# Performance work log

Measured on AMD Instinct MI355X. Metric: run time of the kernel, lower is better.

The kernel has to match this reference:

```python
import jax, jax.numpy as jnp
import numpy as np

BETA = 0.25  # codebook loss weight


def setup_inputs() -> dict:
    key = jax.random.key(0)
    k1, k2 = jax.random.split(key)
    B, C, D = 32768, 4096, 128
    x = jax.random.normal(k1, (B, D), dtype=jnp.float32)
    codes = jax.random.normal(k2, (1, C, D), dtype=jnp.float32)
    return {"x": x, "codes": codes}


def reference(x, codes):
    # x: (B, D), codes: (1, C, D). l2 metric, spherical_norm=False, STE training path
    # (dead-code reinit branch is a no-op on first forward since unused_count==0).
    c = codes[0]  # (C, D)
    x_sq = jnp.sum(x * x, axis=-1, keepdims=True)           # (B, 1)
    c_sq = jnp.sum(c * c, axis=-1)                          # (C,)
    xc = jnp.einsum('bd,cd->bc', x, c)                      # (B, C)
    distances = x_sq + c_sq[None, :] - 2.0 * xc             # (B, C)
    indices = jnp.argmin(distances, axis=-1)                # (B,)
    quantized = c[indices]                                  # (B, D) codebook gather
    # straight-through estimator output
    quantized_out = x + jax.lax.stop_gradient(quantized - x)
    # loss_commit: distance(x, stop_grad(q)); loss_codebook: distance(stop_grad(x), q)
    q_sg = jax.lax.stop_gradient(quantized)
    x_sg = jax.lax.stop_gradient(x)
    loss_commit = jnp.mean(jnp.sum((x - q_sg) ** 2, axis=-1))
    loss_codebook = jnp.mean(jnp.sum((x_sg - quantized) ** 2, axis=-1))
    loss = loss_commit + BETA * loss_codebook
    return quantized_out, indices, loss
```

## Files before the change

### kernel.cpp

```cpp
#include <hip/hip_runtime.h>
#include <float.h>

#define B_ROWS 32768
#define C_CODES 4096
#define DDIM 128
#define MB 128
#define NCHUNKS 2
#define CCHUNK 2048
#define NH 64
#define ROWB 256

typedef __attribute__((ext_vector_type(16))) float f32x16;
using half8 = __attribute__((ext_vector_type(8))) _Float16;
typedef unsigned int u32;
typedef unsigned short u16;
typedef unsigned long long u64;

__device__ __forceinline__ u16 f2h(float f) {
    return __builtin_bit_cast(u16, (_Float16)f);
}

__device__ __forceinline__ void gl2lds16(const void* g, void* l) {
    __builtin_amdgcn_global_load_lds(
        (const __attribute__((address_space(1))) u32*)g,
        (__attribute__((address_space(3))) u32*)l, 16, 0, 0);
}

__global__ void prep_codes(const float* __restrict__ codes, u16* __restrict__ Bbig,
                           float* __restrict__ csqh) {
    const int w = threadIdx.x >> 6, lane = threadIdx.x & 63;
    const int c = blockIdx.x * 4 + w;
    const float2 v = ((const float2*)(codes + (size_t)c * DDIM))[lane];
    ushort2 b; b.x = f2h(v.x); b.y = f2h(v.y);
    const int sw = (c & 15) << 4;
    *(ushort2*)((char*)Bbig + (size_t)c * ROWB + ((lane * 4) ^ sw)) = b;
    float s = v.x * v.x + v.y * v.y;
    #pragma unroll
    for (int off = 32; off; off >>= 1) s += __shfl_xor(s, off);
    if (lane == 0) csqh[c] = 0.5f * s;
}

__global__ void transpose_codes(const float* __restrict__ codes, float* __restrict__ codesT) {
    const int g = blockIdx.x * 256 + threadIdx.x;
    const int d = g & 127;
    const int cg = g >> 7;
    float buf[32];
    #pragma unroll
    for (int k = 0; k < 32; ++k)
        buf[k] = codes[(size_t)(cg * 32 + k) * DDIM + d];
    #pragma unroll
    for (int i = 0; i < 8; ++i) {
        float4 v;
        v.x = buf[i * 4]; v.y = buf[i * 4 + 1]; v.z = buf[i * 4 + 2]; v.w = buf[i * 4 + 3];
        *(float4*)&codesT[(size_t)d * C_CODES + cg * 32 + i * 4] = v;
    }
}

__global__ __launch_bounds__(256, 2)
void gemm_top2(const float* __restrict__ x, const u16* __restrict__ Bbig,
               const float* __restrict__ csqh,
               float* __restrict__ pb1, float* __restrict__ pb2,
               int* __restrict__ pi1, float* __restrict__ xsq2) {
    __shared__ char smem[32768 + 8192];
    char* const Astage = smem;
    float* const csq_l = (float*)(smem + 32768);

    const int tid = threadIdx.x;
    const int lane = tid & 63;
    const int w = tid >> 6;
    const int blkrow = blockIdx.x * MB;
    const int cbase = blockIdx.y * CCHUNK;

    {
        const float4* cs = (const float4*)(csqh + cbase);
        #pragma unroll
        for (int j = 0; j < 2; ++j) {
            const float4 v = cs[j * 256 + tid];
            float4 n; n.x = -v.x; n.y = -v.y; n.z = -v.z; n.w = -v.w;
            ((float4*)csq_l)[j * 256 + tid] = n;
        }
    }
    {
        const int r = tid >> 1, h = tid & 1;
        const float4* xp = (const float4*)(x + (size_t)(blkrow + r) * DDIM + h * 64);
        char* Arow = Astage + r * ROWB;
        const int sw = (r & 15) << 4;
        float ss = 0.f;
        #pragma unroll
        for (int i = 0; i < 16; ++i) {
            const float4 v = xp[i];
            ss += v.x * v.x + v.y * v.y + v.z * v.z + v.w * v.w;
            uint2 pk;
            pk.x = (u32)f2h(v.x) | ((u32)f2h(v.y) << 16);
            pk.y = (u32)f2h(v.z) | ((u32)f2h(v.w) << 16);
            *(uint2*)(Arow + ((h * 128 + i * 8) ^ sw)) = pk;
        }
        if (blockIdx.y == 0) xsq2[blkrow * 2 + tid] = ss;
    }
    __syncthreads();

    const int col0 = lane & 31;
    const int khalf = (lane >> 5) << 4;
    half8 afr[8];
    {
        const int arow = w * 32 + col0;
        const char* Ab = Astage + arow * ROWB;
        const int swa = (arow & 15) << 4;
        #pragma unroll
        for (int ks = 0; ks < 8; ++ks)
            afr[ks] = *(const half8*)(Ab + ((ks * 32 + khalf) ^ swa));
    }
    __syncthreads();

    {
        const char* src = (const char*)Bbig + (size_t)cbase * ROWB;
        gl2lds16(src +         w * 1024 + lane * 16, smem +         w * 1024);
        gl2lds16(src +  4096 + w * 1024 + lane * 16, smem +  4096 + w * 1024);
        gl2lds16(src +  8192 + w * 1024 + lane * 16, smem +  8192 + w * 1024);
        gl2lds16(src + 12288 + w * 1024 + lane * 16, smem + 12288 + w * 1024);
    }
    asm volatile("s_waitcnt vmcnt(2)" ::: "memory");
    __builtin_amdgcn_s_barrier();

    float b1v[16], b2v[16]; int b1i[16];
    #pragma unroll
    for (int r = 0; r < 16; ++r) { b1v[r] = -FLT_MAX; b2v[r] = -FLT_MAX; b1i[r] = 0; }

    const int swb = (col0 & 15) << 4;

    for (int h = 0; h < NH; ++h) {
        if (h + 2 < NH) {
            char* dbuf = smem + ((h + 2) & 3) * 8192;
            const char* src = (const char*)Bbig + (size_t)(cbase + (h + 2) * 32) * ROWB;
            gl2lds16(src +        w * 1024 + lane * 16, dbuf +        w * 1024);
            gl2lds16(src + 4096 + w * 1024 + lane * 16, dbuf + 4096 + w * 1024);
        }
        const char* Bl = smem + (h & 3) * 8192 + col0 * ROWB;

        const float cs0 = csq_l[h * 32 + col0];
        f32x16 acc;
        #pragma unroll
        for (int i = 0; i < 16; ++i) acc[i] = cs0;
        __builtin_amdgcn_s_setprio(1);
        #pragma unroll
        for (int ks = 0; ks < 8; ++ks) {
            const half8 bf = *(const half8*)(Bl + ((ks * 32 + khalf) ^ swb));
            acc = __builtin_amdgcn_mfma_f32_32x32x16_f16(afr[ks], bf, acc, 0, 0, 0);
        }
        __builtin_amdgcn_s_setprio(0);
        const int idx0 = cbase + h * 32 + col0;
        #pragma unroll
        for (int r = 0; r < 16; ++r) {
            const float s0 = acc[r];
            const float m2 = __builtin_amdgcn_fmed3f(b1v[r], b2v[r], s0);
            b1i[r] = (s0 > b1v[r]) ? idx0 : b1i[r];
            b1v[r] = fmaxf(b1v[r], s0);
            b2v[r] = m2;
        }
        if (h + 2 < NH) { asm volatile("s_waitcnt vmcnt(2)" ::: "memory"); }
        else            { asm volatile("s_waitcnt vmcnt(0)" ::: "memory"); }
        __builtin_amdgcn_s_barrier();
    }

    #pragma unroll
    for (int off = 1; off <= 16; off <<= 1) {
        #pragma unroll
        for (int r = 0; r < 16; ++r) {
            const float o1 = __shfl_xor(b1v[r], off);
            const int   oi = __shfl_xor(b1i[r], off);
            const float o2 = __shfl_xor(b2v[r], off);
            const float lo = fminf(b1v[r], o1);
            const float nb2 = fmaxf(lo, fmaxf(b2v[r], o2));
            const bool take = (o1 > b1v[r]) || (o1 == b1v[r] && oi < b1i[r]);
            if (take) { b1v[r] = o1; b1i[r] = oi; }
            b2v[r] = nb2;
        }
    }
    if (col0 == 0) {
        const int hi = lane >> 5;
        #pragma unroll
        for (int r = 0; r < 16; ++r) {
            const int rloc = w * 32 + (r & 3) + 8 * (r >> 2) + 4 * hi;
            const int grow = blkrow + rloc;
            const size_t o = (size_t)blockIdx.y * B_ROWS + grow;
            pb1[o] = b1v[r]; pb2[o] = b2v[r]; pi1[o] = b1i[r];
        }
    }
}

__global__ void select_flag(const float* __restrict__ pb1, const float* __restrict__ pb2,
                            const int* __restrict__ pi1, const float* __restrict__ xsq2,
                            int* __restrict__ idxf, int* __restrict__ list, int* __restrict__ cnt,
                            u64* __restrict__ amax64) {
    const int r = blockIdx.x * 256 + threadIdx.x;
    float b1 = pb1[r], b2 = pb2[r]; int bi = pi1[r];
    #pragma unroll
    for (int c = 1; c < NCHUNKS; ++c) {
        const float o1 = pb1[(size_t)c * B_ROWS + r], o2 = pb2[(size_t)c * B_ROWS + r];
        const int oi = pi1[(size_t)c * B_ROWS + r];
        const float lo = fminf(b1, o1);
        b2 = fmaxf(lo, fmaxf(b2, o2));
        const bool take = (o1 > b1) || (o1 == b1 && oi < bi);
        if (take) { b1 = o1; bi = oi; }
    }
    idxf[r] = bi;
    const float xsq = xsq2[2 * r] + xsq2[2 * r + 1];
    const float margin = 0.004f * sqrtf(xsq) + 0.008f;
    const bool flag = (b1 - b2) < margin;
    const unsigned long long m = __ballot(flag);
    const int lane = threadIdx.x & 63;
    int base = 0;
    const int nw = __popcll(m);
    if (lane == 0 && nw) base = atomicAdd(cnt, nw);
    base = __shfl(base, 0);
    if (flag) {
        const int pos = base + (int)__popcll(m & ((1ull << lane) - 1ull));
        list[pos] = r;
        amax64[pos] = 0ull;
    }
}

__global__ __launch_bounds__(256)
void recheck2(const float* __restrict__ x, const float* __restrict__ codesT,
              const float* __restrict__ csqh, const int* __restrict__ list,
              const int* __restrict__ cnt, u64* __restrict__ amax64) {
    __shared__ float xT[128][8];
    __shared__ u64 warr[4][8];
    const int tid = threadIdx.x;
    const int lane = tid & 63, w = tid >> 6;
    const int n = *cnt;
    if (n == 0) return;
    const int ntasks = ((n + 7) >> 3) << 3;

    for (int task = blockIdx.x; task < ntasks; task += gridDim.x) {
        const int slotbase = (task >> 3) << 3;
        const int ch = task & 7;
        __syncthreads();
        #pragma unroll
        for (int k = 0; k < 4; ++k) {
            const int i = tid + k * 256;
            const int d = i & 127, j = i >> 7;
            const int slot = min(slotbase + j, n - 1);
            xT[d][j] = x[(size_t)list[slot] * DDIM + d];
        }
        __syncthreads();

        const int c0 = ch * 512 + tid;
        const int c1 = c0 + 256;
        float acc[2][8][4];
        #pragma unroll
        for (int cc = 0; cc < 2; ++cc)
            #pragma unroll
            for (int r = 0; r < 8; ++r)
                #pragma unroll
                for (int p = 0; p < 4; ++p) acc[cc][r][p] = 0.f;

        for (int d4 = 0; d4 < 32; ++d4) {
            #pragma unroll
            for (int p = 0; p < 4; ++p) {
                const int d = d4 * 4 + p;
                const float cv0 = codesT[(size_t)d * C_CODES + c0];
                const float cv1 = codesT[(size_t)d * C_CODES + c1];
                const float4 xa = *(const float4*)&xT[d][0];
                const float4 xb = *(const float4*)&xT[d][4];
                acc[0][0][p] = fmaf(cv0, xa.x, acc[0][0][p]);
                acc[0][1][p] = fmaf(cv0, xa.y, acc[0][1][p]);
                acc[0][2][p] = fmaf(cv0, xa.z, acc[0][2][p]);
                acc[0][3][p] = fmaf(cv0, xa.w, acc[0][3][p]);
                acc[0][4][p] = fmaf(cv0, xb.x, acc[0][4][p]);
                acc[0][5][p] = fmaf(cv0, xb.y, acc[0][5][p]);
                acc[0][6][p] = fmaf(cv0, xb.z, acc[0][6][p]);
                acc[0][7][p] = fmaf(cv0, xb.w, acc[0][7][p]);
                acc[1][0][p] = fmaf(cv1, xa.x, acc[1][0][p]);
                acc[1][1][p] = fmaf(cv1, xa.y, acc[1][1][p]);
                acc[1][2][p] = fmaf(cv1, xa.z, acc[1][2][p]);
                acc[1][3][p] = fmaf(cv1, xa.w, acc[1][3][p]);
                acc[1][4][p] = fmaf(cv1, xb.x, acc[1][4][p]);
                acc[1][5][p] = fmaf(cv1, xb.y, acc[1][5][p]);
                acc[1][6][p] = fmaf(cv1, xb.z, acc[1][6][p]);
                acc[1][7][p] = fmaf(cv1, xb.w, acc[1][7][p]);
            }
        }

        const float cq0 = csqh[c0], cq1 = csqh[c1];
        #pragma unroll
        for (int r = 0; r < 8; ++r) {
            const float s0 = (acc[0][r][0] + acc[0][r][1]) + (acc[0][r][2] + acc[0][r][3]) - cq0;
            const float s1 = (acc[1][r][0] + acc[1][r][1]) + (acc[1][r][2] + acc[1][r][3]) - cq1;
            const float sb = (s1 > s0) ? s1 : s0;
            const int ib = (s1 > s0) ? c1 : c0;
            u32 su = __float_as_uint(sb);
            su ^= (sb < 0.f) ? 0xFFFFFFFFu : 0x80000000u;
            u64 key = ((u64)su << 32) | (u32)(4095 - ib);
            #pragma unroll
            for (int off = 1; off < 64; off <<= 1) {
                const u64 o = __shfl_xor(key, off);
                key = (o > key) ? o : key;
            }
            if (lane == 0) warr[w][r] = key;
        }
        __syncthreads();
        if (tid < 8) {
            const u64 k01 = warr[0][tid] > warr[1][tid] ? warr[0][tid] : warr[1][tid];
            const u64 k23 = warr[2][tid] > warr[3][tid] ? warr[2][tid] : warr[3][tid];
            const u64 k = k01 > k23 ? k01 : k23;
            atomicMax(&amax64[min(slotbase + tid, n - 1)], k);
        }
    }
}

__global__ void merge_flag(const int* __restrict__ list, const int* __restrict__ cnt,
                           const u64* __restrict__ amax64, int* __restrict__ idxf) {
    const int n = *cnt;
    for (int i = blockIdx.x * 256 + threadIdx.x; i < n; i += gridDim.x * 256)
        idxf[list[i]] = 4095 - (int)(amax64[i] & 0xFFFFFFFFull);
}

__global__ void finalize(const float* __restrict__ x, const float* __restrict__ codes,
                         const int* __restrict__ idxf, float* __restrict__ qout,
                         float* __restrict__ idxout, float* __restrict__ partials) {
    __shared__ float ls[4];
    const int w = threadIdx.x >> 6, lane = threadIdx.x & 63;
    const int rb = blockIdx.x * 16 + w * 4;
    float wsum = 0.f;
    #pragma unroll
    for (int j = 0; j < 4; ++j) {
        const int r = rb + j;
        const int bi = idxf[r];
        const float2 xv = ((const float2*)(x + (size_t)r * DDIM))[lane];
        const float2 cv = ((const float2*)(codes + (size_t)bi * DDIM))[lane];
        ((float2*)(qout + (size_t)r * DDIM))[lane] = cv;
        if (lane == 0) idxout[r] = (float)bi;
        const float dx = xv.x - cv.x, dy = xv.y - cv.y;
        wsum += dx * dx + dy * dy;
    }
    #pragma unroll
    for (int off = 32; off; off >>= 1) wsum += __shfl_xor(wsum, off);
    if (lane == 0) ls[w] = wsum;
    __syncthreads();
    if (threadIdx.x == 0) partials[blockIdx.x] = (ls[0] + ls[1]) + (ls[2] + ls[3]);
}

__global__ void loss_reduce(const float* __restrict__ partials, float* __restrict__ loss) {
    __shared__ float ls[4];
    const int tid = threadIdx.x, w = tid >> 6, lane = tid & 63;
    float s = 0.f;
    for (int i = tid; i < 2048; i += 256) s += partials[i];
    #pragma unroll
    for (int off = 32; off; off >>= 1) s += __shfl_xor(s, off);
    if (lane == 0) ls[w] = s;
    __syncthreads();
    if (tid == 0) *loss = ((ls[0] + ls[1]) + (ls[2] + ls[3])) * (1.25f / (float)B_ROWS);
}

extern "C" void kernel_launch(void* const* d_in, const int* in_sizes, int n_in,
                              void* d_out, int out_size, void* d_ws, size_t ws_size,
                              hipStream_t stream) {
    const float* x = (const float*)d_in[0];
    const float* codes = (const float*)d_in[1];

    float* out = (float*)d_out;
    float* qout = out;
    float* idxout = out + (size_t)B_ROWS * DDIM;
    float* loss = idxout + B_ROWS;

    float* codesT = qout;

    char* ws = (char*)d_ws;
    u16* Bbig     = (u16*)ws;
    float* csqh   = (float*)(ws + 1048576);
    float* pb1    = (float*)(ws + 1064960);
    float* pb2    = (float*)(ws + 1327104);
    int* pi1      = (int*)(ws + 1589248);
    float* xsq2   = (float*)(ws + 1851392);
    int* idxf     = (int*)(ws + 2113536);
    int* list     = (int*)(ws + 2244608);
    int* cnt      = (int*)(ws + 2375680);
    float* partials = (float*)(ws + 2375808);
    u64* amax64   = (u64*)(ws + 2384000);

    hipMemsetAsync(cnt, 0, 4, stream);
    prep_codes<<<C_CODES / 4, 256, 0, stream>>>(codes, Bbig, csqh);
    transpose_codes<<<64, 256, 0, stream>>>(codes, codesT);
    gemm_top2<<<dim3(B_ROWS / MB, NCHUNKS), 256, 0, stream>>>(x, Bbig, csqh, pb1, pb2, pi1, xsq2);
    select_flag<<<B_ROWS / 256, 256, 0, stream>>>(pb1, pb2, pi1, xsq2, idxf, list, cnt, amax64);
    recheck2<<<2048, 256, 0, stream>>>(x, codesT, csqh, list, cnt, amax64);
    merge_flag<<<64, 256, 0, stream>>>(list, cnt, amax64, idxf);
    finalize<<<B_ROWS / 16, 256, 0, stream>>>(x, codes, idxf, qout, idxout, partials);
    loss_reduce<<<1, 256, 0, stream>>>(partials, loss);
}
```

Baseline: 120.4 us.

## Software-pipeline MFMA tiles with two accumulators to overlap argmax epilogue

Unrolls the codebook tile loop by two and alternates between two accumulator registers, so the argmax/top-2 epilogue of the previous tile runs after the barrier, overlapping with the MFMAs of the next tile. sched_barrier keeps the compiler from reordering across the wait/barrier. The aim is to hide the epilogue's VALU latency behind matrix-core work, at the cost of 16 extra accumulator registers, which may hurt occupancy.

```diff
diff --git a/kernel.cpp b/kernel.cpp
--- a/kernel.cpp
+++ b/kernel.cpp
@@ -128,39 +128,59 @@
 
     const int swb = (col0 & 15) << 4;
 
-    for (int h = 0; h < NH; ++h) {
-        if (h + 2 < NH) {
-            char* dbuf = smem + ((h + 2) & 3) * 8192;
-            const char* src = (const char*)Bbig + (size_t)(cbase + (h + 2) * 32) * ROWB;
-            gl2lds16(src +        w * 1024 + lane * 16, dbuf +        w * 1024);
-            gl2lds16(src + 4096 + w * 1024 + lane * 16, dbuf + 4096 + w * 1024);
-        }
-        const char* Bl = smem + (h & 3) * 8192 + col0 * ROWB;
-
-        const float cs0 = csq_l[h * 32 + col0];
-        f32x16 acc;
-        #pragma unroll
-        for (int i = 0; i < 16; ++i) acc[i] = cs0;
-        __builtin_amdgcn_s_setprio(1);
-        #pragma unroll
-        for (int ks = 0; ks < 8; ++ks) {
-            const half8 bf = *(const half8*)(Bl + ((ks * 32 + khalf) ^ swb));
-            acc = __builtin_amdgcn_mfma_f32_32x32x16_f16(afr[ks], bf, acc, 0, 0, 0);
-        }
-        __builtin_amdgcn_s_setprio(0);
-        const int idx0 = cbase + h * 32 + col0;
-        #pragma unroll
-        for (int r = 0; r < 16; ++r) {
-            const float s0 = acc[r];
-            const float m2 = __builtin_amdgcn_fmed3f(b1v[r], b2v[r], s0);
-            b1i[r] = (s0 > b1v[r]) ? idx0 : b1i[r];
-            b1v[r] = fmaxf(b1v[r], s0);
-            b2v[r] = m2;
-        }
-        if (h + 2 < NH) { asm volatile("s_waitcnt vmcnt(2)" ::: "memory"); }
-        else            { asm volatile("s_waitcnt vmcnt(0)" ::: "memory"); }
-        __builtin_amdgcn_s_barrier();
-    }
+    f32x16 accA, accB;
+
+#define STAGE(hs) do { if ((hs) < NH) { \
+        char* dbuf = smem + ((hs) & 3) * 8192; \
+        const char* src = (const char*)Bbig + (size_t)(cbase + (hs) * 32) * ROWB; \
+        gl2lds16(src +        w * 1024 + lane * 16, dbuf +        w * 1024); \
+        gl2lds16(src + 4096 + w * 1024 + lane * 16, dbuf + 4096 + w * 1024); } } while (0)
+
+#define COMPUTE(h, ACC) do { \
+        const char* Bl = smem + ((h) & 3) * 8192 + col0 * ROWB; \
+        const float cs0 = csq_l[(h) * 32 + col0]; \
+        _Pragma("unroll") \
+        for (int i = 0; i < 16; ++i) ACC[i] = cs0; \
+        __builtin_amdgcn_s_setprio(1); \
+        _Pragma("unroll") \
+        for (int ks = 0; ks < 8; ++ks) { \
+            const half8 bf = *(const half8*)(Bl + ((ks * 32 + khalf) ^ swb)); \
+            ACC = __builtin_amdgcn_mfma_f32_32x32x16_f16(afr[ks], bf, ACC, 0, 0, 0); } \
+        __builtin_amdgcn_s_setprio(0); } while (0)
+
+#define WAITBAR(h) do { \
+        if ((h) + 2 < NH) { asm volatile("s_waitcnt vmcnt(2)" ::: "memory"); } \
+        else              { asm volatile("s_waitcnt vmcnt(0)" ::: "memory"); } \
+        __builtin_amdgcn_s_barrier(); \
+        __builtin_amdgcn_sched_barrier(0); } while (0)
+
+#define EPILOGUE(h, ACC) do { \
+        const int idx0 = cbase + (h) * 32 + col0; \
+        _Pragma("unroll") \
+        for (int r = 0; r < 16; ++r) { \
+            const float s0 = ACC[r]; \
+            const float m2 = __builtin_amdgcn_fmed3f(b1v[r], b2v[r], s0); \
+            b1i[r] = (s0 > b1v[r]) ? idx0 : b1i[r]; \
+            b1v[r] = fmaxf(b1v[r], s0); \
+            b2v[r] = m2; } } while (0)
+
+    for (int h = 0; h < NH; h += 2) {
+        STAGE(h + 2);
+        COMPUTE(h, accA);
+        WAITBAR(h);
+        if (h > 0) EPILOGUE(h - 1, accB);
+
+        STAGE(h + 3);
+        COMPUTE(h + 1, accB);
+        WAITBAR(h + 1);
+        EPILOGUE(h, accA);
+    }
+    EPILOGUE(NH - 1, accB);
+
+#undef STAGE
+#undef COMPUTE
+#undef WAITBAR
+#undef EPILOGUE
 
     #pragma unroll
     for (int off = 1; off <= 16; off <<= 1) {
```

After: 122.1 us. No clear change (+1.4%).
